# Performance work log

Measured on AMD Instinct MI355X. Metric: run time of the kernel, lower is better.

The kernel has to match this reference:

```python
import jax, jax.numpy as jnp
import numpy as np

B, F, C, H, W = 256, 16, 256, 32, 32

def setup_inputs() -> dict:
    key = jax.random.key(0)
    kx, kk = jax.random.split(key)
    x = jax.random.normal(kx, (B, C, H, W), dtype=jnp.float32)
    # kaiming_normal init: std = sqrt(2 / fan_in), fan_in = C*H*W
    std = float(np.sqrt(2.0 / (C * H * W)))
    kernel = jax.random.normal(kk, (F, C, H, W), dtype=jnp.float32) * std
    return {"x": x, "kernel": kernel}

def reference(x, kernel):
    # (x[:,None] * kernel[None]).sum((-1,-2)) == einsum over spatial dims, per channel
    y = jnp.einsum('bchw,fchw->bfc', x, kernel)  # [B, F, C]
    return y.reshape(y.shape[0], -1)  # [B, F*C]
```

## Files before the change

### kernel.cpp

```cpp
#include <hip/hip_runtime.h>
#include <hip/hip_bf16.h>


constexpr int Bb = 256;
constexpr int Ff = 16;
constexpr int Cc = 256;
constexpr int HW = 1024;
constexpr int CHW = Cc * HW;

constexpr int BT = 32;
constexpr int RB = 2;
constexpr int NTHREADS = (BT / RB) * 16;
constexpr int NJ = HW / 4 / 16;

__device__ __forceinline__ float dot4(float4 a, float4 b) {
    return a.x * b.x + a.y * b.y + a.z * b.z + a.w * b.w;
}
__device__ __forceinline__ float red16(float v) {
    v += __shfl_xor(v, 1);
    v += __shfl_xor(v, 2);
    v += __shfl_xor(v, 4);
    v += __shfl_xor(v, 8);
    return v;
}

__global__ __launch_bounds__(NTHREADS)
void sle_kernel(const float* __restrict__ x, const float* __restrict__ k,
                float* __restrict__ out) {
    __shared__ float ldsK[Ff * HW];

    const int t   = threadIdx.x;
    const int thw = t & 15;
    const int tbg = t >> 4;
    const int btile = blockIdx.x & 7;
    const int c     = blockIdx.x >> 3;
    const int b0    = btile * BT + tbg * RB;

    {
        const int fr = t >> 4, lane16 = t & 15;
        const float4* src = (const float4*)(k + (size_t)fr * CHW + (size_t)c * HW);
        float4* dst = (float4*)(ldsK + fr * HW);
#pragma unroll
        for (int q = 0; q < 16; ++q)
            dst[lane16 + 16 * q] = src[lane16 + 16 * q];
    }
    __syncthreads();

    const float* x0 = x + (size_t)(b0 + 0) * CHW + (size_t)c * HW;
    const float* x1 = x + (size_t)(b0 + 1) * CHW + (size_t)c * HW;

    float4 a00 = {0,0,0,0}, a01 = {0,0,0,0}, a02 = {0,0,0,0}, a03 = {0,0,0,0};
    float4 a10 = {0,0,0,0}, a11 = {0,0,0,0}, a12 = {0,0,0,0}, a13 = {0,0,0,0};

#pragma unroll 4
    for (int j = 0; j < NJ; ++j) {
        const int f4  = thw + 16 * j;
        const int off = 4 * f4;
        const float4 xv0 = *(const float4*)(x0 + off);
        const float4 xv1 = *(const float4*)(x1 + off);

#define ACC_G(G, A0, A1) {                                              \
        const float* kp = ldsK + (4 * (G)) * HW + off;                  \
        const float4 k0 = *(const float4*)(kp);                         \
        const float4 k1 = *(const float4*)(kp + HW);                    \
        const float4 k2 = *(const float4*)(kp + 2 * HW);                \
        const float4 k3 = *(const float4*)(kp + 3 * HW);                \
        A0.x += dot4(xv0, k0); A0.y += dot4(xv0, k1);                   \
        A0.z += dot4(xv0, k2); A0.w += dot4(xv0, k3);                   \
        A1.x += dot4(xv1, k0); A1.y += dot4(xv1, k1);                   \
        A1.z += dot4(xv1, k2); A1.w += dot4(xv1, k3); }

        ACC_G(0, a00, a10)
        ACC_G(1, a01, a11)
        ACC_G(2, a02, a12)
        ACC_G(3, a03, a13)
#undef ACC_G
    }

#define RED4(A) { A.x = red16(A.x); A.y = red16(A.y); \
                  A.z = red16(A.z); A.w = red16(A.w); }
    RED4(a00) RED4(a01) RED4(a02) RED4(a03)
    RED4(a10) RED4(a11) RED4(a12) RED4(a13)
#undef RED4

    __syncthreads();
    if (thw == 0) {
        float4* row0 = (float4*)(ldsK + (tbg * RB + 0) * Ff);
        float4* row1 = (float4*)(ldsK + (tbg * RB + 1) * Ff);
        row0[0] = a00; row0[1] = a01; row0[2] = a02; row0[3] = a03;
        row1[0] = a10; row1[1] = a11; row1[2] = a12; row1[3] = a13;
    }
    __syncthreads();

#pragma unroll
    for (int i = 0; i < (BT * Ff) / NTHREADS; ++i) {
        const int idx = t + NTHREADS * i;
        const int bl  = idx >> 4;
        const int f   = idx & 15;
        out[(size_t)(btile * BT + bl) * (Ff * Cc) + f * Cc + c] = ldsK[idx];
    }
}

extern "C" void kernel_launch(void* const* d_in, const int* in_sizes, int n_in,
                              void* d_out, int out_size, void* d_ws, size_t ws_size,
                              hipStream_t stream) {
    const float* x = (const float*)d_in[0];
    const float* k = (const float*)d_in[1];
    float* out = (float*)d_out;
    const int grid = Cc * (Bb / BT);
    sle_kernel<<<grid, NTHREADS, 0, stream>>>(x, k, out);
}
```

Measured before the change: 388.2 us.

## Hold kernel slice in registers and reduce filters with butterfly transpose shuffles

Each thread now keeps all 16 filter float4 values for its spatial slice in registers instead of staging them in LDS. Each block covers one channel and 128 batch rows, with one batch row per loop iteration. The 16 per-filter partial sums are reduced with a halving butterfly of shuffles, so each lane ends up owning one filter, and the wave sums are combined across 4 waves through LDS. This removes the LDS reads of kernel data and the large LDS footprint, but cuts the grid to 512 blocks and puts many shuffles inside the inner loop.

```diff
diff --git a/kernel.cpp b/kernel.cpp
--- a/kernel.cpp
+++ b/kernel.cpp
@@ -1,103 +1,86 @@
 #include <hip/hip_runtime.h>
-#include <hip/hip_bf16.h>
 
 
-constexpr int Bb = 256;
 constexpr int Ff = 16;
 constexpr int Cc = 256;
 constexpr int HW = 1024;
 constexpr int CHW = Cc * HW;
-
-constexpr int BT = 32;
-constexpr int RB = 2;
-constexpr int NTHREADS = (BT / RB) * 16;
-constexpr int NJ = HW / 4 / 16;
+constexpr int NB = 128;
+constexpr int NTHREADS = 256;
+constexpr int NW = 4;
 
 __device__ __forceinline__ float dot4(float4 a, float4 b) {
     return a.x * b.x + a.y * b.y + a.z * b.z + a.w * b.w;
-}
-__device__ __forceinline__ float red16(float v) {
-    v += __shfl_xor(v, 1);
-    v += __shfl_xor(v, 2);
-    v += __shfl_xor(v, 4);
-    v += __shfl_xor(v, 8);
-    return v;
 }
 
 __global__ __launch_bounds__(NTHREADS)
 void sle_kernel(const float* __restrict__ x, const float* __restrict__ k,
                 float* __restrict__ out) {
-    __shared__ float ldsK[Ff * HW];
+    __shared__ float slab[NW * NB * Ff];
 
-    const int t   = threadIdx.x;
-    const int thw = t & 15;
-    const int tbg = t >> 4;
-    const int btile = blockIdx.x & 7;
-    const int c     = blockIdx.x >> 3;
-    const int b0    = btile * BT + tbg * RB;
+    const int t    = threadIdx.x;
+    const int lane = t & 63;
+    const int w    = t >> 6;
+    const int c    = blockIdx.x >> 1;
+    const int b0   = (blockIdx.x & 1) * NB;
+    const int hw0  = 4 * t;
 
-    {
-        const int fr = t >> 4, lane16 = t & 15;
-        const float4* src = (const float4*)(k + (size_t)fr * CHW + (size_t)c * HW);
-        float4* dst = (float4*)(ldsK + fr * HW);
-#pragma unroll
-        for (int q = 0; q < 16; ++q)
-            dst[lane16 + 16 * q] = src[lane16 + 16 * q];
-    }
-    __syncthreads();
+    const float* kb = k + (size_t)c * HW + hw0;
+#define KLD(F) const float4 K##F = *(const float4*)(kb + (F) * CHW);
+    KLD(0)  KLD(1)  KLD(2)  KLD(3)  KLD(4)  KLD(5)  KLD(6)  KLD(7)
+    KLD(8)  KLD(9)  KLD(10) KLD(11) KLD(12) KLD(13) KLD(14) KLD(15)
+#undef KLD
 
-    const float* x0 = x + (size_t)(b0 + 0) * CHW + (size_t)c * HW;
-    const float* x1 = x + (size_t)(b0 + 1) * CHW + (size_t)c * HW;
+    const int fmap = ((lane & 1) << 3) | ((lane & 2) << 1)
+                   | ((lane & 4) >> 1) | ((lane & 8) >> 3);
+    float* myslab = slab + w * (NB * Ff);
+    const bool h1 = lane & 1, h2 = lane & 2, h4 = lane & 4, h8 = lane & 8;
 
-    float4 a00 = {0,0,0,0}, a01 = {0,0,0,0}, a02 = {0,0,0,0}, a03 = {0,0,0,0};
-    float4 a10 = {0,0,0,0}, a11 = {0,0,0,0}, a12 = {0,0,0,0}, a13 = {0,0,0,0};
+    const float* xp = x + (size_t)b0 * CHW + (size_t)c * HW + hw0;
 
 #pragma unroll 4
-    for (int j = 0; j < NJ; ++j) {
-        const int f4  = thw + 16 * j;
-        const int off = 4 * f4;
-        const float4 xv0 = *(const float4*)(x0 + off);
-        const float4 xv1 = *(const float4*)(x1 + off);
+    for (int j = 0; j < NB; ++j) {
+        const float4 xv = *(const float4*)(xp + (size_t)j * CHW);
 
-#define ACC_G(G, A0, A1) {                                              \
-        const float* kp = ldsK + (4 * (G)) * HW + off;                  \
-        const float4 k0 = *(const float4*)(kp);                         \
-        const float4 k1 = *(const float4*)(kp + HW);                    \
-        const float4 k2 = *(const float4*)(kp + 2 * HW);                \
-        const float4 k3 = *(const float4*)(kp + 3 * HW);                \
-        A0.x += dot4(xv0, k0); A0.y += dot4(xv0, k1);                   \
-        A0.z += dot4(xv0, k2); A0.w += dot4(xv0, k3);                   \
-        A1.x += dot4(xv1, k0); A1.y += dot4(xv1, k1);                   \
-        A1.z += dot4(xv1, k2); A1.w += dot4(xv1, k3); }
+        const float s0  = dot4(xv, K0),  s1  = dot4(xv, K1);
+        const float s2  = dot4(xv, K2),  s3  = dot4(xv, K3);
+        const float s4  = dot4(xv, K4),  s5  = dot4(xv, K5);
+        const float s6  = dot4(xv, K6),  s7  = dot4(xv, K7);
+        const float s8  = dot4(xv, K8),  s9  = dot4(xv, K9);
+        const float s10 = dot4(xv, K10), s11 = dot4(xv, K11);
+        const float s12 = dot4(xv, K12), s13 = dot4(xv, K13);
+        const float s14 = dot4(xv, K14), s15 = dot4(xv, K15);
 
-        ACC_G(0, a00, a10)
-        ACC_G(1, a01, a11)
-        ACC_G(2, a02, a12)
-        ACC_G(3, a03, a13)
-#undef ACC_G
+#define HALVE(OUT, A, B, H, M) \
+        const float OUT = ((H) ? (B) : (A)) + __shfl_xor(((H) ? (A) : (B)), (M));
+        HALVE(t0, s0, s8,  h1, 1) HALVE(t1, s1, s9,  h1, 1)
+        HALVE(t2, s2, s10, h1, 1) HALVE(t3, s3, s11, h1, 1)
+        HALVE(t4, s4, s12, h1, 1) HALVE(t5, s5, s13, h1, 1)
+        HALVE(t6, s6, s14, h1, 1) HALVE(t7, s7, s15, h1, 1)
+        HALVE(u0, t0, t4, h2, 2) HALVE(u1, t1, t5, h2, 2)
+        HALVE(u2, t2, t6, h2, 2) HALVE(u3, t3, t7, h2, 2)
+        HALVE(v0, u0, u2, h4, 4) HALVE(v1, u1, u3, h4, 4)
+        HALVE(r0, v0, v1, h8, 8)
+#undef HALVE
+        float r = r0;
+        r += __shfl_xor(r, 16);
+        r += __shfl_xor(r, 32);
+
+        if (lane < 16) myslab[j * Ff + fmap] = r;
     }
 
-#define RED4(A) { A.x = red16(A.x); A.y = red16(A.y); \
-                  A.z = red16(A.z); A.w = red16(A.w); }
-    RED4(a00) RED4(a01) RED4(a02) RED4(a03)
-    RED4(a10) RED4(a11) RED4(a12) RED4(a13)
-#undef RED4
-
-    __syncthreads();
-    if (thw == 0) {
-        float4* row0 = (float4*)(ldsK + (tbg * RB + 0) * Ff);
-        float4* row1 = (float4*)(ldsK + (tbg * RB + 1) * Ff);
-        row0[0] = a00; row0[1] = a01; row0[2] = a02; row0[3] = a03;
-        row1[0] = a10; row1[1] = a11; row1[2] = a12; row1[3] = a13;
-    }
     __syncthreads();
 
 #pragma unroll
-    for (int i = 0; i < (BT * Ff) / NTHREADS; ++i) {
+    for (int i = 0; i < (NB * Ff) / NTHREADS; ++i) {
         const int idx = t + NTHREADS * i;
-        const int bl  = idx >> 4;
-        const int f   = idx & 15;
-        out[(size_t)(btile * BT + bl) * (Ff * Cc) + f * Cc + c] = ldsK[idx];
+        const float s = slab[idx]
+                      + slab[idx + 1 * NB * Ff]
+                      + slab[idx + 2 * NB * Ff]
+                      + slab[idx + 3 * NB * Ff];
+        const int jb = idx >> 4;
+        const int f  = idx & 15;
+        out[(size_t)(b0 + jb) * (Ff * Cc) + f * Cc + c] = s;
     }
 }
 
@@ -107,6 +90,5 @@
     const float* x = (const float*)d_in[0];
     const float* k = (const float*)d_in[1];
     float* out = (float*)d_out;
-    const int grid = Cc * (Bb / BT);
-    sle_kernel<<<grid, NTHREADS, 0, stream>>>(x, k, out);
+    sle_kernel<<<Cc * 2, NTHREADS, 0, stream>>>(x, k, out);
 }
```

New measurement: 419.7 us. 1.08x slower.
